# Kernel tuning notes

Measured on AMD Instinct MI355X. Metric: run time of the kernel, lower is better.

## Reference

```python
import jax, jax.numpy as jnp
import numpy as np

N, HIDDEN, HEADS, HEAD = 20000, 128, 8, 16
LAP, NBUCKETS, NBINS, MAXDEG, E = 16, 1024, 32, 64, 320000


def _mlp(x, W1, b1, W2, b2):
    return jax.nn.relu(x @ W1 + b1) @ W2 + b2


def _build_pairs(bq, bk, edge_index):
    """Host-side: P_LSH = {(i,j)!=: bq[i]==bk[j]} union graph edges, deduped.
    Mirrors _lsh_pairs + torch.unique (data-dependent size -> numpy)."""
    bq = np.asarray(bq); bk = np.asarray(bk); ei = np.asarray(edge_index)
    srcs = [ei[0].astype(np.int64)]; dsts = [ei[1].astype(np.int64)]
    common = np.intersect1d(np.unique(bq), np.unique(bk))
    for b in common:
        qn = np.nonzero(bq == b)[0]
        kn = np.nonzero(bk == b)[0]
        ii = np.repeat(qn, kn.size)
        jj = np.tile(kn, qn.size)
        m = ii != jj
        srcs.append(ii[m].astype(np.int64)); dsts.append(jj[m].astype(np.int64))
    src = np.concatenate(srcs); dst = np.concatenate(dsts)
    code = np.unique(src * np.int64(N) + dst)  # dedup pairs
    return jnp.asarray(code // N, jnp.int32), jnp.asarray(code % N, jnp.int32)


def setup_inputs() -> dict:
    key = jax.random.key(0)
    ks = jax.random.split(key, 16)
    rn = lambda k, sh, s=1.0: (jax.random.normal(k, sh, jnp.float32) * s)
    d_in = HIDDEN + LAP
    return {
        "Q": rn(ks[0], (N, HIDDEN)),
        "K": rn(ks[1], (N, HIDDEN)),
        "V": rn(ks[2], (N, HIDDEN)),
        "lap_pe": jax.random.uniform(ks[3], (N, LAP), jnp.float32),
        "W_q1": rn(ks[4], (d_in, HIDDEN), d_in ** -0.5), "b_q1": jnp.zeros((HIDDEN,), jnp.float32),
        "W_q2": rn(ks[5], (HIDDEN, NBUCKETS), HIDDEN ** -0.5), "b_q2": jnp.zeros((NBUCKETS,), jnp.float32),
        "W_k1": rn(ks[6], (d_in, HIDDEN), d_in ** -0.5), "b_k1": jnp.zeros((HIDDEN,), jnp.float32),
        "W_k2": rn(ks[7], (HIDDEN, NBUCKETS), HIDDEN ** -0.5), "b_k2": jnp.zeros((NBUCKETS,), jnp.float32),
        "spd_bias": rn(ks[8], (NBINS + 1, HEADS), 0.02),
        "deg_src_emb": rn(ks[9], (MAXDEG + 2, HEADS), 0.02),
        "deg_dst_emb": rn(ks[10], (MAXDEG + 2, HEADS), 0.02),
        "W_out": rn(ks[11], (HIDDEN, HIDDEN), HIDDEN ** -0.5), "b_out": jnp.zeros((HIDDEN,), jnp.float32),
        "spd_boundaries": jnp.linspace(0.0, 2.0, NBINS).astype(jnp.float32),
        "edge_index": jax.random.randint(ks[12], (2, E), 0, N, jnp.int32),
        "deg": jax.random.randint(ks[13], (N,), 0, MAXDEG + 1, jnp.int32),
    }


def reference(Q, K, V, lap_pe, W_q1, b_q1, W_q2, b_q2, W_k1, b_k1, W_k2, b_k2,
              spd_bias, deg_src_emb, deg_dst_emb, W_out, b_out, spd_boundaries,
              edge_index, deg):
    q_in = jnp.concatenate([Q, lap_pe], axis=-1)
    k_in = jnp.concatenate([K, lap_pe], axis=-1)
    l_q = _mlp(q_in, W_q1, b_q1, W_q2, b_q2)  # (N, B)
    l_k = _mlp(k_in, W_k1, b_k1, W_k2, b_k2)
    src, dst = _build_pairs(jnp.argmax(l_q, -1), jnp.argmax(l_k, -1), edge_index)

    Qh = Q.reshape(N, HEADS, HEAD)
    Kh = K.reshape(N, HEADS, HEAD)
    Vh = V.reshape(N, HEADS, HEAD)

    scores = jnp.einsum("ehd,ehd->eh", Qh[src], Kh[dst]) / (HEAD ** 0.5)  # (P, H)
    pe_dist = jnp.linalg.norm(lap_pe[src] - lap_pe[dst], axis=-1)
    spd_idx = jnp.searchsorted(spd_boundaries, pe_dist, side="left")  # torch.bucketize(right=False)
    scores = scores + spd_bias[spd_idx]
    dsrc = jnp.clip(deg[src], 0, MAXDEG + 1)
    ddst = jnp.clip(deg[dst], 0, MAXDEG + 1)
    scores = scores + deg_src_emb[dsrc] + deg_dst_emb[ddst]

    # pyg_softmax: segment softmax over src index
    m = jax.ops.segment_max(scores, src, num_segments=N)  # (N, H)
    m = jnp.where(jnp.isneginf(m), 0.0, m)
    ex = jnp.exp(scores - m[src])
    denom = jax.ops.segment_sum(ex, src, num_segments=N)
    alpha = ex / (denom[src] + 1e-16)  # dropout p=0 (eval)

    h = jax.ops.segment_sum(alpha[..., None] * Vh[dst], src, num_segments=N)
    h_global = h.reshape(N, HIDDEN) @ W_out + b_out
    return h_global, l_q, l_k
```

## Files before the change

kernel.cpp:

```cpp
#include <hip/hip_runtime.h>
#include <math.h>

#define NN 20000
#define HID 128
#define NH 8
#define HD 16
#define LAPD 16
#define NB 1024
#define NBINS 32
#define MAXDEG 64
#define NE 320000
#define DIN 144

#define NEGH (-1.0e30f)

__global__ __launch_bounds__(256) void mlp_kernel(
    const float* __restrict__ X, const float* __restrict__ lap,
    const float* __restrict__ W1, const float* __restrict__ b1,
    const float* __restrict__ W2, const float* __restrict__ b2,
    float* __restrict__ outL, int* __restrict__ bidx)
{
    __shared__ __align__(16) float xs[16][DIN];
    __shared__ __align__(16) float hs[16][HID];
    __shared__ float rbv[64];
    __shared__ int   rbi[64];
    const int tid = threadIdx.x;
    const int n0 = blockIdx.x * 16;

    for (int e = tid; e < 16 * DIN; e += 256) {
        int n = e / DIN, k = e - n * DIN;
        float v = (k < HID) ? X[(size_t)(n0 + n) * HID + k]
                            : lap[(size_t)(n0 + n) * LAPD + (k - HID)];
        xs[n][k] = v;
    }
    __syncthreads();

    const int c = tid & 127, ng = tid >> 7;
    float hacc[8];
    {
        float bb = b1[c];
        #pragma unroll
        for (int m = 0; m < 8; m++) hacc[m] = bb;
        for (int k = 0; k < DIN; k += 4) {
            float w0 = W1[(k + 0) * HID + c];
            float w1 = W1[(k + 1) * HID + c];
            float w2 = W1[(k + 2) * HID + c];
            float w3 = W1[(k + 3) * HID + c];
            #pragma unroll
            for (int m = 0; m < 8; m++) {
                float4 xv = *(const float4*)&xs[ng * 8 + m][k];
                hacc[m] = fmaf(xv.x, w0, hacc[m]);
                hacc[m] = fmaf(xv.y, w1, hacc[m]);
                hacc[m] = fmaf(xv.z, w2, hacc[m]);
                hacc[m] = fmaf(xv.w, w3, hacc[m]);
            }
        }
    }
    #pragma unroll
    for (int m = 0; m < 8; m++) hs[ng * 8 + m][c] = fmaxf(hacc[m], 0.0f);
    __syncthreads();

    float acc[4][16];
    #pragma unroll
    for (int c4 = 0; c4 < 4; c4++)
        #pragma unroll
        for (int m = 0; m < 16; m++) acc[c4][m] = 0.0f;

    for (int k = 0; k < HID; k += 4) {
        float w[4][4];
        #pragma unroll
        for (int kk = 0; kk < 4; kk++)
            #pragma unroll
            for (int c4 = 0; c4 < 4; c4++)
                w[kk][c4] = W2[(size_t)(k + kk) * NB + c4 * 256 + tid];
        #pragma unroll
        for (int m = 0; m < 16; m++) {
            float4 hv = *(const float4*)&hs[m][k];
            #pragma unroll
            for (int c4 = 0; c4 < 4; c4++) {
                acc[c4][m] = fmaf(hv.x, w[0][c4], acc[c4][m]);
                acc[c4][m] = fmaf(hv.y, w[1][c4], acc[c4][m]);
                acc[c4][m] = fmaf(hv.z, w[2][c4], acc[c4][m]);
                acc[c4][m] = fmaf(hv.w, w[3][c4], acc[c4][m]);
            }
        }
    }

    float bb4[4];
    #pragma unroll
    for (int c4 = 0; c4 < 4; c4++) bb4[c4] = b2[c4 * 256 + tid];

    const int lane = tid & 63, wv = tid >> 6;
    for (int m = 0; m < 16; m++) {
        float bv = -3.0e38f; int bi = 0x7fffffff;
        #pragma unroll
        for (int c4 = 0; c4 < 4; c4++) {
            int o = c4 * 256 + tid;
            float v = acc[c4][m] + bb4[c4];
            outL[(size_t)(n0 + m) * NB + o] = v;
            if (v > bv || (v == bv && o < bi)) { bv = v; bi = o; }
        }
        #pragma unroll
        for (int off = 1; off < 64; off <<= 1) {
            float ov = __shfl_xor(bv, off, 64);
            int   oi = __shfl_xor(bi, off, 64);
            if (ov > bv || (ov == bv && oi < bi)) { bv = ov; bi = oi; }
        }
        if (lane == 0) { rbv[wv * 16 + m] = bv; rbi[wv * 16 + m] = bi; }
    }
    __syncthreads();
    if (tid < 16) {
        float bv = rbv[tid]; int bi = rbi[tid];
        #pragma unroll
        for (int ww = 1; ww < 4; ww++) {
            float ov = rbv[ww * 16 + tid]; int oi = rbi[ww * 16 + tid];
            if (ov > bv || (ov == bv && oi < bi)) { bv = ov; bi = oi; }
        }
        bidx[n0 + tid] = min(max(bi, 0), NB - 1);
    }
}

__global__ void zero_kernel(int* __restrict__ p, int n) {
    int i = blockIdx.x * 256 + threadIdx.x;
    if (i < n) p[i] = 0;
}

__global__ void hist_kernel(const int* __restrict__ bkarr, int* __restrict__ bcnt) {
    int i = blockIdx.x * 256 + threadIdx.x;
    if (i < NN) {
        int b = min(max(bkarr[i], 0), NB - 1);
        atomicAdd(&bcnt[b], 1);
    }
}

__global__ __launch_bounds__(1024) void scan_bucket_kernel(const int* __restrict__ cnt,
        int* __restrict__ off, int* __restrict__ fill) {
    __shared__ int s[1024];
    int t = threadIdx.x;
    int v = cnt[t];
    s[t] = v; __syncthreads();
    for (int o = 1; o < 1024; o <<= 1) {
        int a = (t >= o) ? s[t - o] : 0;
        __syncthreads();
        s[t] += a;
        __syncthreads();
    }
    int excl = s[t] - v;
    off[t] = excl; fill[t] = excl;
    if (t == 1023) off[NB] = s[1023];
}

__global__ __launch_bounds__(1024) void scan_edge_kernel(const int* __restrict__ cnt,
        int* __restrict__ off, int* __restrict__ fill) {
    __shared__ int s[1024];
    const int t = threadIdx.x;
    const int base = t * 20;
    int loc[20]; int sum = 0;
    #pragma unroll
    for (int k = 0; k < 20; k++) {
        int idx = base + k;
        int v = (idx < NN) ? cnt[idx] : 0;
        loc[k] = sum; sum += v;
    }
    s[t] = sum; __syncthreads();
    for (int o = 1; o < 1024; o <<= 1) {
        int a = (t >= o) ? s[t - o] : 0;
        __syncthreads();
        s[t] += a;
        __syncthreads();
    }
    int pre = s[t] - sum;
    #pragma unroll
    for (int k = 0; k < 20; k++) {
        int idx = base + k;
        if (idx < NN) { int e = pre + loc[k]; off[idx] = e; fill[idx] = e; }
    }
    if (t == 1023) off[NN] = s[1023];
}

__global__ void scatter_bucket_kernel(const int* __restrict__ bkarr,
        int* __restrict__ fill, int* __restrict__ blist) {
    int i = blockIdx.x * 256 + threadIdx.x;
    if (i < NN) {
        int b = min(max(bkarr[i], 0), NB - 1);
        int p = atomicAdd(&fill[b], 1);
        if (p >= 0 && p < NN) blist[p] = i;
    }
}

__global__ void edge_count_kernel(const int* __restrict__ ei, int* __restrict__ ecnt) {
    int e = blockIdx.x * 256 + threadIdx.x;
    if (e < NE) {
        int s = min(max(ei[e], 0), NN - 1);
        atomicAdd(&ecnt[s], 1);
    }
}

__global__ void edge_scatter_kernel(const int* __restrict__ ei,
        int* __restrict__ fill, int* __restrict__ adj) {
    int e = blockIdx.x * 256 + threadIdx.x;
    if (e < NE) {
        int s = min(max(ei[e], 0), NN - 1);
        int d = min(max(ei[NE + e], 0), NN - 1);
        int p = atomicAdd(&fill[s], 1);
        if (p >= 0 && p < NE) adj[p] = d;
    }
}

__global__ __launch_bounds__(64) void attn_kernel(
    const float* __restrict__ Q, const float* __restrict__ K, const float* __restrict__ V,
    const float* __restrict__ lap,
    const float* __restrict__ spdb, const float* __restrict__ dse,
    const float* __restrict__ dde, const float* __restrict__ bndr,
    const int* __restrict__ deg,
    const int* __restrict__ bq, const int* __restrict__ bkarr,
    const int* __restrict__ boff, const int* __restrict__ blist,
    const int* __restrict__ eoff, const int* __restrict__ adj,
    const float* __restrict__ Wout, const float* __restrict__ bout,
    float* __restrict__ outH)
{
    __shared__ float qf[128];
    __shared__ float pef[16];
    __shared__ float bnd[32];
    __shared__ float red[64][33];
    __shared__ float hsm[128];
    const int i = blockIdx.x;
    const int lane = threadIdx.x;

    qf[lane]      = Q[(size_t)i * HID + lane];
    qf[lane + 64] = Q[(size_t)i * HID + 64 + lane];
    if (lane < 16) pef[lane] = lap[(size_t)i * LAPD + lane];
    if (lane < 32) bnd[lane] = bndr[lane];

    int b = min(max(bq[i], 0), NB - 1);
    int bs = boff[b], be = boff[b + 1];
    bs = min(max(bs, 0), NN); be = min(max(be, bs), NN);
    int es = eoff[i], ee = eoff[i + 1];
    es = min(max(es, 0), NE); ee = min(max(ee, es), NE);
    const int Lb = be - bs;
    const int Ltot = Lb + (ee - es);
    const int degi = min(max(deg[i], 0), MAXDEG + 1);
    __syncthreads();

    float dsrc[8];
    #pragma unroll
    for (int h = 0; h < 8; h++) dsrc[h] = dse[degi * 8 + h];

    float m8[8], l8[8], acc[128];
    #pragma unroll
    for (int h = 0; h < 8; h++) { m8[h] = NEGH; l8[h] = 0.0f; }
    #pragma unroll
    for (int cidx = 0; cidx < 128; cidx++) acc[cidx] = 0.0f;

    for (int t0 = 0; t0 < Ltot; t0 += 64) {
        const int t = t0 + lane;
        int j = 0; bool valid = false;
        if (t < Ltot) {
            if (t < Lb) {
                j = blist[bs + t];
                j = min(max(j, 0), NN - 1);
                valid = (j != i);
            } else {
                const int p = t - Lb;
                j = adj[es + p];
                j = min(max(j, 0), NN - 1);
                valid = (j == i) || (bkarr[j] != b);
                if (valid) {
                    for (int q = 0; q < p; q++)
                        if (adj[es + q] == j) { valid = false; break; }
                }
            }
        }
        float s8[8];
        if (valid) {
            const float4* K4 = (const float4*)(K + (size_t)j * HID);
            #pragma unroll
            for (int h = 0; h < 8; h++) {
                float4 k0 = K4[h * 4 + 0], k1 = K4[h * 4 + 1];
                float4 k2 = K4[h * 4 + 2], k3 = K4[h * 4 + 3];
                float dot = 0.0f;
                dot = fmaf(qf[h*16+ 0], k0.x, dot); dot = fmaf(qf[h*16+ 1], k0.y, dot);
                dot = fmaf(qf[h*16+ 2], k0.z, dot); dot = fmaf(qf[h*16+ 3], k0.w, dot);
                dot = fmaf(qf[h*16+ 4], k1.x, dot); dot = fmaf(qf[h*16+ 5], k1.y, dot);
                dot = fmaf(qf[h*16+ 6], k1.z, dot); dot = fmaf(qf[h*16+ 7], k1.w, dot);
                dot = fmaf(qf[h*16+ 8], k2.x, dot); dot = fmaf(qf[h*16+ 9], k2.y, dot);
                dot = fmaf(qf[h*16+10], k2.z, dot); dot = fmaf(qf[h*16+11], k2.w, dot);
                dot = fmaf(qf[h*16+12], k3.x, dot); dot = fmaf(qf[h*16+13], k3.y, dot);
                dot = fmaf(qf[h*16+14], k3.z, dot); dot = fmaf(qf[h*16+15], k3.w, dot);
                s8[h] = dot * 0.25f;
            }
            const float* lj = lap + (size_t)j * LAPD;
            float ss = 0.0f;
            #pragma unroll
            for (int d = 0; d < 16; d++) { float df = pef[d] - lj[d]; ss = fmaf(df, df, ss); }
            float dist = sqrtf(ss);
            int si = 0;
            #pragma unroll
            for (int kb = 0; kb < 32; kb++) si += (bnd[kb] < dist) ? 1 : 0;
            const int dj = min(max(deg[j], 0), MAXDEG + 1);
            #pragma unroll
            for (int h = 0; h < 8; h++)
                s8[h] += spdb[si * 8 + h] + dsrc[h] + dde[dj * 8 + h];
        } else {
            #pragma unroll
            for (int h = 0; h < 8; h++) s8[h] = NEGH;
        }

        float alpha8[8];
        #pragma unroll
        for (int h = 0; h < 8; h++) {
            float cm = s8[h];
            #pragma unroll
            for (int off = 1; off < 64; off <<= 1)
                cm = fmaxf(cm, __shfl_xor(cm, off, 64));
            const float mn = fmaxf(m8[h], cm);
            alpha8[h] = __expf(m8[h] - mn);
            const float p = valid ? __expf(s8[h] - mn) : 0.0f;
            l8[h] = l8[h] * alpha8[h] + p;
            m8[h] = mn;
            s8[h] = p;
        }

        const float4* V4 = (const float4*)(V + (size_t)j * HID);
        #pragma unroll
        for (int h = 0; h < 8; h++) {
            float4 v0, v1, v2, v3;
            if (valid) {
                v0 = V4[h * 4 + 0]; v1 = V4[h * 4 + 1];
                v2 = V4[h * 4 + 2]; v3 = V4[h * 4 + 3];
            } else {
                v0 = v1 = v2 = v3 = make_float4(0.f, 0.f, 0.f, 0.f);
            }
            const float p = s8[h], al = alpha8[h];
            float* a = &acc[h * 16];
            a[ 0] = fmaf(p, v0.x, a[ 0] * al); a[ 1] = fmaf(p, v0.y, a[ 1] * al);
            a[ 2] = fmaf(p, v0.z, a[ 2] * al); a[ 3] = fmaf(p, v0.w, a[ 3] * al);
            a[ 4] = fmaf(p, v1.x, a[ 4] * al); a[ 5] = fmaf(p, v1.y, a[ 5] * al);
            a[ 6] = fmaf(p, v1.z, a[ 6] * al); a[ 7] = fmaf(p, v1.w, a[ 7] * al);
            a[ 8] = fmaf(p, v2.x, a[ 8] * al); a[ 9] = fmaf(p, v2.y, a[ 9] * al);
            a[10] = fmaf(p, v2.z, a[10] * al); a[11] = fmaf(p, v2.w, a[11] * al);
            a[12] = fmaf(p, v3.x, a[12] * al); a[13] = fmaf(p, v3.y, a[13] * al);
            a[14] = fmaf(p, v3.z, a[14] * al); a[15] = fmaf(p, v3.w, a[15] * al);
        }
    }

    #pragma unroll
    for (int h = 0; h < 8; h++) {
        float v = l8[h];
        #pragma unroll
        for (int off = 1; off < 64; off <<= 1) v += __shfl_xor(v, off, 64);
        l8[h] = 1.0f / (v + 1e-16f);
    }

    const int cc = lane & 31, half = lane >> 5;
    #pragma unroll
    for (int g = 0; g < 4; g++) {
        __syncthreads();
        #pragma unroll
        for (int k = 0; k < 32; k++) red[lane][k] = acc[g * 32 + k];
        __syncthreads();
        float v = 0.0f;
        #pragma unroll
        for (int jj = 0; jj < 32; jj++) v += red[half * 32 + jj][cc];
        v += __shfl_xor(v, 32, 64);
        if (half == 0) {
            const int cidx = g * 32 + cc;
            hsm[cidx] = v * l8[cidx >> 4];
        }
    }
    __syncthreads();

    float o0 = bout[lane];
    float o1 = bout[lane + 64];
    for (int k = 0; k < HID; k++) {
        const float hk = hsm[k];
        o0 = fmaf(hk, Wout[k * HID + lane], o0);
        o1 = fmaf(hk, Wout[k * HID + 64 + lane], o1);
    }
    outH[(size_t)i * HID + lane]      = o0;
    outH[(size_t)i * HID + 64 + lane] = o1;
}

extern "C" void kernel_launch(void* const* d_in, const int* in_sizes, int n_in,
                              void* d_out, int out_size, void* d_ws, size_t ws_size,
                              hipStream_t stream) {
    const float* Q    = (const float*)d_in[0];
    const float* Kx   = (const float*)d_in[1];
    const float* Vx   = (const float*)d_in[2];
    const float* lap  = (const float*)d_in[3];
    const float* Wq1  = (const float*)d_in[4];
    const float* bq1  = (const float*)d_in[5];
    const float* Wq2  = (const float*)d_in[6];
    const float* bq2  = (const float*)d_in[7];
    const float* Wk1  = (const float*)d_in[8];
    const float* bk1  = (const float*)d_in[9];
    const float* Wk2  = (const float*)d_in[10];
    const float* bk2  = (const float*)d_in[11];
    const float* spdb = (const float*)d_in[12];
    const float* dse  = (const float*)d_in[13];
    const float* dde  = (const float*)d_in[14];
    const float* Wout = (const float*)d_in[15];
    const float* bout = (const float*)d_in[16];
    const float* bndr = (const float*)d_in[17];
    const int*   ei   = (const int*)d_in[18];
    const int*   deg  = (const int*)d_in[19];

    float* out   = (float*)d_out;
    float* outH  = out;
    float* outLq = out + (size_t)NN * HID;
    float* outLk = outLq + (size_t)NN * NB;

    int* wsp = (int*)d_ws;
    size_t o = 0;
    auto carve = [&](size_t n_ints) -> int* {
        int* p = wsp + o; o += n_ints; return p;
    };
    int* bcnt  = carve(NB);
    int* boff  = carve(NB + 1);
    int* bfill = carve(NB);
    int* blist = carve(NN);
    int* bqv   = carve(NN);
    int* bkv   = carve(NN);
    int* ecnt  = carve(NN);
    int* eoff  = carve(NN + 1);
    int* efill = carve(NN);
    int* adj   = carve(NE);

    zero_kernel<<<(NB + 255) / 256, 256, 0, stream>>>(bcnt, NB);
    zero_kernel<<<(NN + 255) / 256, 256, 0, stream>>>(ecnt, NN);

    mlp_kernel<<<NN / 16, 256, 0, stream>>>(Q,  lap, Wq1, bq1, Wq2, bq2, outLq, bqv);
    mlp_kernel<<<NN / 16, 256, 0, stream>>>(Kx, lap, Wk1, bk1, Wk2, bk2, outLk, bkv);

    hist_kernel<<<(NN + 255) / 256, 256, 0, stream>>>(bkv, bcnt);
    scan_bucket_kernel<<<1, 1024, 0, stream>>>(bcnt, boff, bfill);
    scatter_bucket_kernel<<<(NN + 255) / 256, 256, 0, stream>>>(bkv, bfill, blist);

    edge_count_kernel<<<(NE + 255) / 256, 256, 0, stream>>>(ei, ecnt);
    scan_edge_kernel<<<1, 1024, 0, stream>>>(ecnt, eoff, efill);
    edge_scatter_kernel<<<(NE + 255) / 256, 256, 0, stream>>>(ei, efill, adj);

    attn_kernel<<<NN, 64, 0, stream>>>(Q, Kx, Vx, lap, spdb, dse, dde, bndr, deg,
                                       bqv, bkv, boff, blist, eoff, adj,
                                       Wout, bout, outH);
}
```

Baseline: 988.3 us.

## Restructure attention V accumulation to column-per-lane and vectorize MLP logits

The attention kernel no longer keeps a 128-float accumulator per lane, which had to be reduced across lanes through shared memory at the end. Softmax weights are now staged in shared memory, and each lane accumulates two output columns by streaming V rows for every candidate in the chunk. This cuts register pressure and removes the final reduction, at the cost of extra barriers, wave-wide sum shuffles per head, and serialized V row loads. The kernel also caches bias tables in LDS, vectorizes the q loads, and asks for higher occupancy via launch bounds. Separately, the MLP second layer switches to float4 W2 loads and float4 logit stores, which changes each thread's column mapping to contiguous groups of four.

Result: slower. 1.023 ms (+3.5%).

```diff
diff --git a/kernel.cpp b/kernel.cpp
--- a/kernel.cpp
+++ b/kernel.cpp
@@ -60,51 +60,42 @@
     for (int m = 0; m < 8; m++) hs[ng * 8 + m][c] = fmaxf(hacc[m], 0.0f);
     __syncthreads();
 
-    float acc[4][16];
-    #pragma unroll
-    for (int c4 = 0; c4 < 4; c4++)
-        #pragma unroll
-        for (int m = 0; m < 16; m++) acc[c4][m] = 0.0f;
+    float a0[16], a1[16], a2[16], a3[16];
+    #pragma unroll
+    for (int m = 0; m < 16; m++) { a0[m] = 0.f; a1[m] = 0.f; a2[m] = 0.f; a3[m] = 0.f; }
 
     for (int k = 0; k < HID; k += 4) {
-        float w[4][4];
-        #pragma unroll
-        for (int kk = 0; kk < 4; kk++)
-            #pragma unroll
-            for (int c4 = 0; c4 < 4; c4++)
-                w[kk][c4] = W2[(size_t)(k + kk) * NB + c4 * 256 + tid];
+        const float4 w0 = *(const float4*)&W2[(size_t)(k + 0) * NB + 4 * tid];
+        const float4 w1 = *(const float4*)&W2[(size_t)(k + 1) * NB + 4 * tid];
+        const float4 w2 = *(const float4*)&W2[(size_t)(k + 2) * NB + 4 * tid];
+        const float4 w3 = *(const float4*)&W2[(size_t)(k + 3) * NB + 4 * tid];
         #pragma unroll
         for (int m = 0; m < 16; m++) {
-            float4 hv = *(const float4*)&hs[m][k];
-            #pragma unroll
-            for (int c4 = 0; c4 < 4; c4++) {
-                acc[c4][m] = fmaf(hv.x, w[0][c4], acc[c4][m]);
-                acc[c4][m] = fmaf(hv.y, w[1][c4], acc[c4][m]);
-                acc[c4][m] = fmaf(hv.z, w[2][c4], acc[c4][m]);
-                acc[c4][m] = fmaf(hv.w, w[3][c4], acc[c4][m]);
-            }
-        }
-    }
-
-    float bb4[4];
-    #pragma unroll
-    for (int c4 = 0; c4 < 4; c4++) bb4[c4] = b2[c4 * 256 + tid];
-
+            const float4 hv = *(const float4*)&hs[m][k];
+            a0[m] = fmaf(hv.x, w0.x, fmaf(hv.y, w1.x, fmaf(hv.z, w2.x, fmaf(hv.w, w3.x, a0[m]))));
+            a1[m] = fmaf(hv.x, w0.y, fmaf(hv.y, w1.y, fmaf(hv.z, w2.y, fmaf(hv.w, w3.y, a1[m]))));
+            a2[m] = fmaf(hv.x, w0.z, fmaf(hv.y, w1.z, fmaf(hv.z, w2.z, fmaf(hv.w, w3.z, a2[m]))));
+            a3[m] = fmaf(hv.x, w0.w, fmaf(hv.y, w1.w, fmaf(hv.z, w2.w, fmaf(hv.w, w3.w, a3[m]))));
+        }
+    }
+
+    const float4 bb4 = *(const float4*)&b2[4 * tid];
     const int lane = tid & 63, wv = tid >> 6;
+    const int o0 = 4 * tid;
     for (int m = 0; m < 16; m++) {
-        float bv = -3.0e38f; int bi = 0x7fffffff;
-        #pragma unroll
-        for (int c4 = 0; c4 < 4; c4++) {
-            int o = c4 * 256 + tid;
-            float v = acc[c4][m] + bb4[c4];
-            outL[(size_t)(n0 + m) * NB + o] = v;
-            if (v > bv || (v == bv && o < bi)) { bv = v; bi = o; }
-        }
+        float4 ov;
+        ov.x = a0[m] + bb4.x; ov.y = a1[m] + bb4.y;
+        ov.z = a2[m] + bb4.z; ov.w = a3[m] + bb4.w;
+        *(float4*)&outL[(size_t)(n0 + m) * NB + o0] = ov;
+        float bv = ov.x; int bi = o0;
+        if (ov.y > bv) { bv = ov.y; bi = o0 + 1; }
+        if (ov.z > bv) { bv = ov.z; bi = o0 + 2; }
+        if (ov.w > bv) { bv = ov.w; bi = o0 + 3; }
         #pragma unroll
         for (int off = 1; off < 64; off <<= 1) {
-            float ov = __shfl_xor(bv, off, 64);
-            int   oi = __shfl_xor(bi, off, 64);
-            if (ov > bv || (ov == bv && oi < bi)) { bv = ov; bi = oi; }
+            float ovv = __shfl_xor(bv, off, 64);
+            int   oi  = __shfl_xor(bi, off, 64);
+            if (ovv > bv || (ovv == bv && oi < bi)) { bv = ovv; bi = oi; }
         }
         if (lane == 0) { rbv[wv * 16 + m] = bv; rbi[wv * 16 + m] = bi; }
     }
@@ -207,7 +198,7 @@
     }
 }
 
-__global__ __launch_bounds__(64) void attn_kernel(
+__global__ __launch_bounds__(64, 4) void attn_kernel(
     const float* __restrict__ Q, const float* __restrict__ K, const float* __restrict__ V,
     const float* __restrict__ lap,
     const float* __restrict__ spdb, const float* __restrict__ dse,
@@ -219,18 +210,27 @@
     const float* __restrict__ Wout, const float* __restrict__ bout,
     float* __restrict__ outH)
 {
-    __shared__ float qf[128];
+    __shared__ __align__(16) float qf[128];
     __shared__ float pef[16];
     __shared__ float bnd[32];
-    __shared__ float red[64][33];
+    __shared__ int   jls[64];
+    __shared__ float wtsT[8][65];
+    __shared__ float al8[8];
+    __shared__ float lsum[8];
     __shared__ float hsm[128];
+    __shared__ float spdbs[(NBINS + 1) * NH];
+    __shared__ float ddes[(MAXDEG + 2) * NH];
     const int i = blockIdx.x;
     const int lane = threadIdx.x;
+    const int h0 = lane >> 4;
+    const int h1 = h0 + 4;
 
     qf[lane]      = Q[(size_t)i * HID + lane];
     qf[lane + 64] = Q[(size_t)i * HID + 64 + lane];
     if (lane < 16) pef[lane] = lap[(size_t)i * LAPD + lane];
     if (lane < 32) bnd[lane] = bndr[lane];
+    for (int e = lane; e < (NBINS + 1) * NH; e += 64) spdbs[e] = spdb[e];
+    for (int e = lane; e < (MAXDEG + 2) * NH; e += 64) ddes[e] = dde[e];
 
     int b = min(max(bq[i], 0), NB - 1);
     int bs = boff[b], be = boff[b + 1];
@@ -246,11 +246,10 @@
     #pragma unroll
     for (int h = 0; h < 8; h++) dsrc[h] = dse[degi * 8 + h];
 
-    float m8[8], l8[8], acc[128];
+    float m8[8], l8[8];
     #pragma unroll
     for (int h = 0; h < 8; h++) { m8[h] = NEGH; l8[h] = 0.0f; }
-    #pragma unroll
-    for (int cidx = 0; cidx < 128; cidx++) acc[cidx] = 0.0f;
+    float acc0 = 0.0f, acc1 = 0.0f;
 
     for (int t0 = 0; t0 < Ltot; t0 += 64) {
         const int t = t0 + lane;
@@ -271,6 +270,8 @@
                 }
             }
         }
+        jls[lane] = valid ? j : 0;
+
         float s8[8];
         if (valid) {
             const float4* K4 = (const float4*)(K + (size_t)j * HID);
@@ -278,15 +279,19 @@
             for (int h = 0; h < 8; h++) {
                 float4 k0 = K4[h * 4 + 0], k1 = K4[h * 4 + 1];
                 float4 k2 = K4[h * 4 + 2], k3 = K4[h * 4 + 3];
+                float4 q0 = *(const float4*)&qf[h * 16 + 0];
+                float4 q1 = *(const float4*)&qf[h * 16 + 4];
+                float4 q2 = *(const float4*)&qf[h * 16 + 8];
+                float4 q3 = *(const float4*)&qf[h * 16 + 12];
                 float dot = 0.0f;
-                dot = fmaf(qf[h*16+ 0], k0.x, dot); dot = fmaf(qf[h*16+ 1], k0.y, dot);
-                dot = fmaf(qf[h*16+ 2], k0.z, dot); dot = fmaf(qf[h*16+ 3], k0.w, dot);
-                dot = fmaf(qf[h*16+ 4], k1.x, dot); dot = fmaf(qf[h*16+ 5], k1.y, dot);
-                dot = fmaf(qf[h*16+ 6], k1.z, dot); dot = fmaf(qf[h*16+ 7], k1.w, dot);
-                dot = fmaf(qf[h*16+ 8], k2.x, dot); dot = fmaf(qf[h*16+ 9], k2.y, dot);
-                dot = fmaf(qf[h*16+10], k2.z, dot); dot = fmaf(qf[h*16+11], k2.w, dot);
-                dot = fmaf(qf[h*16+12], k3.x, dot); dot = fmaf(qf[h*16+13], k3.y, dot);
-                dot = fmaf(qf[h*16+14], k3.z, dot); dot = fmaf(qf[h*16+15], k3.w, dot);
+                dot = fmaf(q0.x, k0.x, dot); dot = fmaf(q0.y, k0.y, dot);
+                dot = fmaf(q0.z, k0.z, dot); dot = fmaf(q0.w, k0.w, dot);
+                dot = fmaf(q1.x, k1.x, dot); dot = fmaf(q1.y, k1.y, dot);
+                dot = fmaf(q1.z, k1.z, dot); dot = fmaf(q1.w, k1.w, dot);
+                dot = fmaf(q2.x, k2.x, dot); dot = fmaf(q2.y, k2.y, dot);
+                dot = fmaf(q2.z, k2.z, dot); dot = fmaf(q2.w, k2.w, dot);
+                dot = fmaf(q3.x, k3.x, dot); dot = fmaf(q3.y, k3.y, dot);
+                dot = fmaf(q3.z, k3.z, dot); dot = fmaf(q3.w, k3.w, dot);
                 s8[h] = dot * 0.25f;
             }
             const float* lj = lap + (size_t)j * LAPD;
@@ -300,7 +305,7 @@
             const int dj = min(max(deg[j], 0), MAXDEG + 1);
             #pragma unroll
             for (int h = 0; h < 8; h++)
-                s8[h] += spdb[si * 8 + h] + dsrc[h] + dde[dj * 8 + h];
+                s8[h] += spdbs[si * 8 + h] + dsrc[h] + ddes[dj * 8 + h];
         } else {
             #pragma unroll
             for (int h = 0; h < 8; h++) s8[h] = NEGH;
@@ -315,59 +320,46 @@
                 cm = fmaxf(cm, __shfl_xor(cm, off, 64));
             const float mn = fmaxf(m8[h], cm);
             alpha8[h] = __expf(m8[h] - mn);
-            const float p = valid ? __expf(s8[h] - mn) : 0.0f;
-            l8[h] = l8[h] * alpha8[h] + p;
+            float p = valid ? __expf(s8[h] - mn) : 0.0f;
+            float sp = p;
+            #pragma unroll
+            for (int off = 1; off < 64; off <<= 1)
+                sp += __shfl_xor(sp, off, 64);
+            l8[h] = l8[h] * alpha8[h] + sp;
             m8[h] = mn;
-            s8[h] = p;
-        }
-
-        const float4* V4 = (const float4*)(V + (size_t)j * HID);
-        #pragma unroll
-        for (int h = 0; h < 8; h++) {
-            float4 v0, v1, v2, v3;
-            if (valid) {
-                v0 = V4[h * 4 + 0]; v1 = V4[h * 4 + 1];
-                v2 = V4[h * 4 + 2]; v3 = V4[h * 4 + 3];
-            } else {
-                v0 = v1 = v2 = v3 = make_float4(0.f, 0.f, 0.f, 0.f);
-            }
-            const float p = s8[h], al = alpha8[h];
-            float* a = &acc[h * 16];
-            a[ 0] = fmaf(p, v0.x, a[ 0] * al); a[ 1] = fmaf(p, v0.y, a[ 1] * al);
-            a[ 2] = fmaf(p, v0.z, a[ 2] * al); a[ 3] = fmaf(p, v0.w, a[ 3] * al);
-            a[ 4] = fmaf(p, v1.x, a[ 4] * al); a[ 5] = fmaf(p, v1.y, a[ 5] * al);
-            a[ 6] = fmaf(p, v1.z, a[ 6] * al); a[ 7] = fmaf(p, v1.w, a[ 7] * al);
-            a[ 8] = fmaf(p, v2.x, a[ 8] * al); a[ 9] = fmaf(p, v2.y, a[ 9] * al);
-            a[10] = fmaf(p, v2.z, a[10] * al); a[11] = fmaf(p, v2.w, a[11] * al);
-            a[12] = fmaf(p, v3.x, a[12] * al); a[13] = fmaf(p, v3.y, a[13] * al);
-            a[14] = fmaf(p, v3.z, a[14] * al); a[15] = fmaf(p, v3.w, a[15] * al);
-        }
-    }
-
-    #pragma unroll
-    for (int h = 0; h < 8; h++) {
-        float v = l8[h];
-        #pragma unroll
-        for (int off = 1; off < 64; off <<= 1) v += __shfl_xor(v, off, 64);
-        l8[h] = 1.0f / (v + 1e-16f);
-    }
-
-    const int cc = lane & 31, half = lane >> 5;
-    #pragma unroll
-    for (int g = 0; g < 4; g++) {
-        __syncthreads();
-        #pragma unroll
-        for (int k = 0; k < 32; k++) red[lane][k] = acc[g * 32 + k];
-        __syncthreads();
-        float v = 0.0f;
-        #pragma unroll
-        for (int jj = 0; jj < 32; jj++) v += red[half * 32 + jj][cc];
-        v += __shfl_xor(v, 32, 64);
-        if (half == 0) {
-            const int cidx = g * 32 + cc;
-            hsm[cidx] = v * l8[cidx >> 4];
-        }
-    }
+            wtsT[h][lane] = p;
+        }
+        if (lane == 0) {
+            #pragma unroll
+            for (int h = 0; h < 8; h++) al8[h] = alpha8[h];
+        }
+        __syncthreads();
+
+        acc0 *= al8[h0];
+        acc1 *= al8[h1];
+        const int rem = Ltot - t0;
+        const int nc = (rem >= 64) ? 64 : ((rem + 7) & ~7);
+        #pragma unroll 8
+        for (int cc = 0; cc < nc; ++cc) {
+            const int jc = __builtin_amdgcn_readfirstlane(jls[cc]);
+            const float w0 = wtsT[h0][cc];
+            const float w1 = wtsT[h1][cc];
+            const float* vr = V + (size_t)jc * HID;
+            acc0 = fmaf(w0, vr[lane], acc0);
+            acc1 = fmaf(w1, vr[lane + 64], acc1);
+        }
+        __syncthreads();
+    }
+
+    if (lane == 0) {
+        #pragma unroll
+        for (int h = 0; h < 8; h++) lsum[h] = l8[h];
+    }
+    __syncthreads();
+    const float linv0 = 1.0f / (lsum[h0] + 1e-16f);
+    const float linv1 = 1.0f / (lsum[h1] + 1e-16f);
+    hsm[lane]      = acc0 * linv0;
+    hsm[lane + 64] = acc1 * linv1;
     __syncthreads();
 
     float o0 = bout[lane];
```
